# Optimization experiments

Hardware: AMD Instinct MI355X
Metric: run time of the kernel (lower is better)

The kernel has to match this reference:

```python
import jax, jax.numpy as jnp
import numpy as np

B, W, Q = 64, 128, 256
H, A, C = 512, 128, 20
SCALE = 0.05  # keep gates out of saturation


def setup_inputs() -> dict:
    key = jax.random.key(0)
    ks = jax.random.split(key, 9)
    return {
        "quantized_repr": jax.random.normal(ks[0], (B, W, Q), jnp.float32),
        "w_in": jax.random.normal(ks[1], (H, Q), jnp.float32) * SCALE,
        "b_in": jax.random.normal(ks[2], (H,), jnp.float32) * SCALE,
        "w_ih": jax.random.normal(ks[3], (4 * H, A), jnp.float32) * SCALE,
        "w_hh": jax.random.normal(ks[4], (4 * H, H), jnp.float32) * SCALE,
        "b_ih": jax.random.normal(ks[5], (4 * H,), jnp.float32) * SCALE,
        "b_hh": jax.random.normal(ks[6], (4 * H,), jnp.float32) * SCALE,
        "w_out": jax.random.normal(ks[7], (A, H), jnp.float32) * SCALE,
        "b_out": jax.random.normal(ks[8], (A,), jnp.float32) * SCALE,
        "max_char_len": C,
    }


def reference(quantized_repr, w_in, b_in, w_ih, w_hh, b_ih, b_hh, w_out, b_out, max_char_len):
    b, w, q = quantized_repr.shape
    hdim = w_hh.shape[1]
    vocab = w_out.shape[0]
    dt = quantized_repr.dtype

    # input_projection -> initial hidden, zero cell, flattened over (B*W)
    h0 = (quantized_repr @ w_in.T + b_in).reshape(b * w, hdim)
    c0 = jnp.zeros_like(h0)
    x0 = jax.nn.one_hot(jnp.zeros((b * w,), jnp.int32), vocab, dtype=dt)  # <start> = char 0
    bias = b_ih + b_hh

    def step(carry, _):
        h, c, x = carry
        gates = x @ w_ih.T + h @ w_hh.T + bias  # [BW, 4H]
        i, f, g, o = jnp.split(gates, 4, axis=-1)  # torch gate order i,f,g,o
        i = jax.nn.sigmoid(i)
        f = jax.nn.sigmoid(f)
        g = jnp.tanh(g)
        o = jax.nn.sigmoid(o)
        c = f * c + i * g
        h = o * jnp.tanh(c)
        logits = h @ w_out.T + b_out  # [BW, A]
        x_next = jax.nn.one_hot(jnp.argmax(logits, axis=-1), vocab, dtype=dt)
        return (h, c, x_next), logits

    _, logits = jax.lax.scan(step, (h0, c0, x0), None, length=max_char_len)  # [C, BW, A]
    return logits.transpose(1, 0, 2).reshape(b, w, max_char_len, vocab)
```

## Files before the change

### kernel.cpp

```cpp
#include <hip/hip_runtime.h>
#include <math.h>

typedef float fv4 __attribute__((ext_vector_type(4)));

#define NSTEP 20
#define HD 512
#define QD 256
#define VOC 128
#define RB 16
#define TPB 512

#define WG_OFF   0
#define WIH_OFF  1048576
#define WIN_OFF  1310720
#define WOUT_OFF 1441792

__device__ __forceinline__ float sig_np(float x) {
  float t = (float)exp(-(double)x);
  return __fdiv_rn(1.0f, __fadd_rn(1.0f, t));
}
__device__ __forceinline__ float tanh_np(float x) {
  return (float)tanh((double)x);
}

__global__ void repack_kernel(const float* __restrict__ w_in,
                              const float* __restrict__ w_ih,
                              const float* __restrict__ w_hh,
                              const float* __restrict__ w_out,
                              float* __restrict__ ws) {
  int t = blockIdx.x * blockDim.x + threadIdx.x;
  {
    int ki = t & 3, u = (t >> 2) & 511, g = (t >> 11) & 3, kb = t >> 13;
    ws[WG_OFF + t] = w_hh[(size_t)(g * HD + u) * HD + kb * 4 + ki];
  }
  if (t < 262144) {
    int u = t & 511, g = (t >> 9) & 3, x = t >> 11;
    ws[WIH_OFF + t] = w_ih[(size_t)(g * HD + u) * VOC + x];
  }
  if (t < 131072) {
    int ki = t & 3, u = (t >> 2) & 511, kb = t >> 11;
    ws[WIN_OFF + t] = w_in[(size_t)u * QD + kb * 4 + ki];
  }
  if (t < 65536) {
    int ki = t & 3, v = (t >> 2) & 127, kb = t >> 9;
    ws[WOUT_OFF + t] = w_out[(size_t)v * HD + kb * 4 + ki];
  }
}

__global__ __launch_bounds__(TPB, 2)
void decoder_fast(const float* __restrict__ quant,
                  const float* __restrict__ b_in,
                  const float* __restrict__ b_ih,
                  const float* __restrict__ b_hh,
                  const float* __restrict__ b_out,
                  const float* __restrict__ ws,
                  float* __restrict__ out) {
  __shared__ __align__(16) float hLDS[RB * HD];
  __shared__ __align__(16) float scratch[RB * QD];
  __shared__ int idxLDS[RB];

  const int tid  = threadIdx.x;
  const int row0 = blockIdx.x * RB;

  const fv4* Wg4   = (const fv4*)(ws + WG_OFF);
  const float* Wih = ws + WIH_OFF;
  const fv4* Win4  = (const fv4*)(ws + WIN_OFF);
  const fv4* Wout4 = (const fv4*)(ws + WOUT_OFF);
  const fv4* hLDS4 = (const fv4*)hLDS;
  const fv4* q4    = (const fv4*)scratch;

  {
    const fv4* src = (const fv4*)(quant + (size_t)row0 * QD);
    fv4* dst = (fv4*)scratch;
    dst[tid]       = src[tid];
    dst[tid + TPB] = src[tid + TPB];
  }
  if (tid < RB) idxLDS[tid] = 0;

  float bias[4];
#pragma unroll
  for (int g = 0; g < 4; ++g)
    bias[g] = __fadd_rn(b_ih[g * HD + tid], b_hh[g * HD + tid]);
  const float bout = b_out[tid & (VOC - 1)];
  const float binu = b_in[tid];

  __syncthreads();

  {
    float a[RB];
#pragma unroll
    for (int r = 0; r < RB; ++r) a[r] = 0.0f;
    for (int kb = 0; kb < QD / 4; ++kb) {
      fv4 w = Win4[kb * 512 + tid];
#pragma unroll
      for (int r = 0; r < RB; ++r) {
        fv4 qv = q4[r * 64 + kb];
        a[r] = __builtin_fmaf(w[0], qv[0], a[r]);
        a[r] = __builtin_fmaf(w[1], qv[1], a[r]);
        a[r] = __builtin_fmaf(w[2], qv[2], a[r]);
        a[r] = __builtin_fmaf(w[3], qv[3], a[r]);
      }
    }
#pragma unroll
    for (int r = 0; r < RB; ++r) hLDS[r * HD + tid] = __fadd_rn(a[r], binu);
  }

  float c[RB];
#pragma unroll
  for (int r = 0; r < RB; ++r) c[r] = 0.0f;

  __syncthreads();

  for (int t = 0; t < NSTEP; ++t) {
    float acc[RB][4];
#pragma unroll
    for (int r = 0; r < RB; ++r)
#pragma unroll
      for (int g = 0; g < 4; ++g) acc[r][g] = 0.0f;

    for (int kb = 0; kb < HD / 4; ++kb) {
      fv4 wv[4];
#pragma unroll
      for (int g = 0; g < 4; ++g) wv[g] = Wg4[(kb * 4 + g) * 512 + tid];
#pragma unroll
      for (int r = 0; r < RB; ++r) {
        fv4 hv = hLDS4[r * 128 + kb];
#pragma unroll
        for (int g = 0; g < 4; ++g) {
          acc[r][g] = __builtin_fmaf(wv[g][0], hv[0], acc[r][g]);
          acc[r][g] = __builtin_fmaf(wv[g][1], hv[1], acc[r][g]);
          acc[r][g] = __builtin_fmaf(wv[g][2], hv[2], acc[r][g]);
          acc[r][g] = __builtin_fmaf(wv[g][3], hv[3], acc[r][g]);
        }
      }
    }

    float hnew[RB];
#pragma unroll
    for (int r = 0; r < RB; ++r) {
      int ix = idxLDS[r];
      float ga[4];
#pragma unroll
      for (int g = 0; g < 4; ++g) {
        float t1 = Wih[(ix * 4 + g) * 512 + tid];
        ga[g] = __fadd_rn(__fadd_rn(t1, acc[r][g]), bias[g]);
      }
      float ig = sig_np(ga[0]);
      float fg = sig_np(ga[1]);
      float gg = tanh_np(ga[2]);
      float og = sig_np(ga[3]);
      c[r] = __fadd_rn(__fmul_rn(fg, c[r]), __fmul_rn(ig, gg));
      hnew[r] = __fmul_rn(og, tanh_np(c[r]));
    }
    __syncthreads();
#pragma unroll
    for (int r = 0; r < RB; ++r) hLDS[r * HD + tid] = hnew[r];
    __syncthreads();

    {
      int v = tid & (VOC - 1), rq = tid >> 7;
      float la[4];
#pragma unroll
      for (int j = 0; j < 4; ++j) la[j] = 0.0f;
      for (int kb = 0; kb < HD / 4; ++kb) {
        fv4 wv = Wout4[kb * 128 + v];
#pragma unroll
        for (int j = 0; j < 4; ++j) {
          fv4 hv = hLDS4[(rq * 4 + j) * 128 + kb];
          la[j] = __builtin_fmaf(wv[0], hv[0], la[j]);
          la[j] = __builtin_fmaf(wv[1], hv[1], la[j]);
          la[j] = __builtin_fmaf(wv[2], hv[2], la[j]);
          la[j] = __builtin_fmaf(wv[3], hv[3], la[j]);
        }
      }
      float* lg = scratch;
#pragma unroll
      for (int j = 0; j < 4; ++j) {
        int r = rq * 4 + j;
        float val = __fadd_rn(la[j], bout);
        lg[r * VOC + v] = val;
        out[(size_t)((row0 + r) * NSTEP + t) * VOC + v] = val;
      }
    }
    __syncthreads();

    if (tid < RB) {
      const float* lg = scratch + tid * VOC;
      float mv = lg[0];
      int mi = 0;
      for (int v = 1; v < VOC; ++v) {
        float x = lg[v];
        if (x > mv) { mv = x; mi = v; }
      }
      idxLDS[tid] = mi;
    }
    __syncthreads();
  }
}

extern "C" void kernel_launch(void* const* d_in, const int* in_sizes, int n_in,
                              void* d_out, int out_size, void* d_ws, size_t ws_size,
                              hipStream_t stream) {
  const float* quant = (const float*)d_in[0];
  const float* w_in  = (const float*)d_in[1];
  const float* b_in  = (const float*)d_in[2];
  const float* w_ih  = (const float*)d_in[3];
  const float* w_hh  = (const float*)d_in[4];
  const float* b_ih  = (const float*)d_in[5];
  const float* b_hh  = (const float*)d_in[6];
  const float* w_out = (const float*)d_in[7];
  const float* b_out = (const float*)d_in[8];
  float* out = (float*)d_out;
  float* ws  = (float*)d_ws;

  repack_kernel<<<4096, 256, 0, stream>>>(w_in, w_ih, w_hh, w_out, ws);
  decoder_fast<<<8192 / RB, TPB, 0, stream>>>(quant, b_in, b_ih, b_hh, b_out,
                                              ws, out);
}
```

Measured before the change: 7.098 ms.

## Fuse output projection into next step's gate GEMM and use wave-shuffle argmax

The kernel computes the logits for step t-1 inside the step-t gate matmul loop, since both read the same h vectors from LDS, which removes a separate pass over hLDS and two barriers per step. Argmax becomes a 64-lane shuffle reduction per wave, with a two-wave candidate merge through LDS, replacing a serial 128-element scan by 16 threads. Most of the cell state moves from registers to LDS (14 rows in LDS, 2 in registers) to cut register pressure, and the row order is rotated per thread group to spread LDS accesses. Biases are reloaded every step and a final logits pass is added after the loop; the extra LDS traffic for c and the larger loop body may offset the savings.

Measured after the change: 5.993 ms. -15.6%, faster.

```diff
diff --git a/kernel.cpp b/kernel.cpp
--- a/kernel.cpp
+++ b/kernel.cpp
@@ -9,6 +9,8 @@
 #define VOC 128
 #define RB 16
 #define TPB 512
+#define CREG 2
+#define CLDSROWS (RB - CREG)
 
 #define WG_OFF   0
 #define WIH_OFF  1048576
@@ -56,145 +58,168 @@
                   const float* __restrict__ ws,
                   float* __restrict__ out) {
   __shared__ __align__(16) float hLDS[RB * HD];
-  __shared__ __align__(16) float scratch[RB * QD];
-  __shared__ int idxLDS[RB];
+  __shared__ __align__(16) float cLDS[CLDSROWS * HD];
+  __shared__ float2 cand[RB][2];
 
   const int tid  = threadIdx.x;
   const int row0 = blockIdx.x * RB;
+  const int v    = tid & (VOC - 1);
+  const int rqs  = (tid >> 7) << 2;
+  const int wpar = (tid >> 6) & 1;
 
   const fv4* Wg4   = (const fv4*)(ws + WG_OFF);
   const float* Wih = ws + WIH_OFF;
   const fv4* Win4  = (const fv4*)(ws + WIN_OFF);
   const fv4* Wout4 = (const fv4*)(ws + WOUT_OFF);
   const fv4* hLDS4 = (const fv4*)hLDS;
-  const fv4* q4    = (const fv4*)scratch;
 
   {
     const fv4* src = (const fv4*)(quant + (size_t)row0 * QD);
-    fv4* dst = (fv4*)scratch;
+    fv4* dst = (fv4*)hLDS;
     dst[tid]       = src[tid];
     dst[tid + TPB] = src[tid + TPB];
   }
-  if (tid < RB) idxLDS[tid] = 0;
-
-  float bias[4];
-#pragma unroll
-  for (int g = 0; g < 4; ++g)
-    bias[g] = __fadd_rn(b_ih[g * HD + tid], b_hh[g * HD + tid]);
-  const float bout = b_out[tid & (VOC - 1)];
-  const float binu = b_in[tid];
-
   __syncthreads();
 
-  {
-    float a[RB];
-#pragma unroll
-    for (int r = 0; r < RB; ++r) a[r] = 0.0f;
+  float a0[RB];
+  {
+    const fv4* q4 = (const fv4*)hLDS;
+#pragma unroll
+    for (int r = 0; r < RB; ++r) a0[r] = 0.0f;
     for (int kb = 0; kb < QD / 4; ++kb) {
       fv4 w = Win4[kb * 512 + tid];
 #pragma unroll
       for (int r = 0; r < RB; ++r) {
         fv4 qv = q4[r * 64 + kb];
-        a[r] = __builtin_fmaf(w[0], qv[0], a[r]);
-        a[r] = __builtin_fmaf(w[1], qv[1], a[r]);
-        a[r] = __builtin_fmaf(w[2], qv[2], a[r]);
-        a[r] = __builtin_fmaf(w[3], qv[3], a[r]);
-      }
-    }
-#pragma unroll
-    for (int r = 0; r < RB; ++r) hLDS[r * HD + tid] = __fadd_rn(a[r], binu);
-  }
-
-  float c[RB];
-#pragma unroll
-  for (int r = 0; r < RB; ++r) c[r] = 0.0f;
-
+        a0[r] = __builtin_fmaf(w[0], qv[0], a0[r]);
+        a0[r] = __builtin_fmaf(w[1], qv[1], a0[r]);
+        a0[r] = __builtin_fmaf(w[2], qv[2], a0[r]);
+        a0[r] = __builtin_fmaf(w[3], qv[3], a0[r]);
+      }
+    }
+  }
+  const float binu = b_in[tid];
   __syncthreads();
+#pragma unroll
+  for (int r = 0; r < RB; ++r) hLDS[r * HD + tid] = __fadd_rn(a0[r], binu);
+  __syncthreads();
+
+  float cR0 = 0.0f, cR1 = 0.0f;
 
   for (int t = 0; t < NSTEP; ++t) {
     float acc[RB][4];
-#pragma unroll
-    for (int r = 0; r < RB; ++r)
-#pragma unroll
-      for (int g = 0; g < 4; ++g) acc[r][g] = 0.0f;
+    float la[4];
+#pragma unroll
+    for (int rr = 0; rr < RB; ++rr)
+#pragma unroll
+      for (int g = 0; g < 4; ++g) acc[rr][g] = 0.0f;
+#pragma unroll
+    for (int j = 0; j < 4; ++j) la[j] = 0.0f;
 
     for (int kb = 0; kb < HD / 4; ++kb) {
       fv4 wv[4];
 #pragma unroll
       for (int g = 0; g < 4; ++g) wv[g] = Wg4[(kb * 4 + g) * 512 + tid];
-#pragma unroll
-      for (int r = 0; r < RB; ++r) {
+      fv4 wvo = Wout4[kb * 128 + v];
+#pragma unroll
+      for (int rr = 0; rr < RB; ++rr) {
+        const int r = (rr + rqs) & (RB - 1);
         fv4 hv = hLDS4[r * 128 + kb];
 #pragma unroll
         for (int g = 0; g < 4; ++g) {
-          acc[r][g] = __builtin_fmaf(wv[g][0], hv[0], acc[r][g]);
-          acc[r][g] = __builtin_fmaf(wv[g][1], hv[1], acc[r][g]);
-          acc[r][g] = __builtin_fmaf(wv[g][2], hv[2], acc[r][g]);
-          acc[r][g] = __builtin_fmaf(wv[g][3], hv[3], acc[r][g]);
+          acc[rr][g] = __builtin_fmaf(wv[g][0], hv[0], acc[rr][g]);
+          acc[rr][g] = __builtin_fmaf(wv[g][1], hv[1], acc[rr][g]);
+          acc[rr][g] = __builtin_fmaf(wv[g][2], hv[2], acc[rr][g]);
+          acc[rr][g] = __builtin_fmaf(wv[g][3], hv[3], acc[rr][g]);
         }
-      }
-    }
-
-    float hnew[RB];
-#pragma unroll
-    for (int r = 0; r < RB; ++r) {
-      int ix = idxLDS[r];
+        if (rr < 4) {
+          la[rr] = __builtin_fmaf(wvo[0], hv[0], la[rr]);
+          la[rr] = __builtin_fmaf(wvo[1], hv[1], la[rr]);
+          la[rr] = __builtin_fmaf(wvo[2], hv[2], la[rr]);
+          la[rr] = __builtin_fmaf(wvo[3], hv[3], la[rr]);
+        }
+      }
+    }
+
+    if (t > 0) {
+      const float boutv = b_out[v];
+#pragma unroll
+      for (int j = 0; j < 4; ++j) {
+        float val = __fadd_rn(la[j], boutv);
+        out[(size_t)((row0 + rqs + j) * NSTEP + (t - 1)) * VOC + v] = val;
+        float mv = val;
+        int   mi = v;
+#pragma unroll
+        for (int m = 1; m < 64; m <<= 1) {
+          float ov = __shfl_xor(mv, m);
+          int   oi = __shfl_xor(mi, m);
+          bool take = (ov > mv) || (ov == mv && oi < mi);
+          mv = take ? ov : mv;
+          mi = take ? oi : mi;
+        }
+        if ((tid & 63) == 0)
+          cand[rqs + j][wpar] = make_float2(mv, __int_as_float(mi));
+      }
+    }
+    __syncthreads();
+
+    float biasg[4];
+#pragma unroll
+    for (int g = 0; g < 4; ++g)
+      biasg[g] = __fadd_rn(b_ih[g * HD + tid], b_hh[g * HD + tid]);
+
+#pragma unroll
+    for (int rr = 0; rr < RB; ++rr) {
+      const int r = (rr + rqs) & (RB - 1);
+      int ix = 0;
+      if (t > 0) {
+        float2 c0 = cand[r][0], c1 = cand[r][1];
+        ix = (c1.x > c0.x) ? __float_as_int(c1.y) : __float_as_int(c0.y);
+      }
       float ga[4];
 #pragma unroll
       for (int g = 0; g < 4; ++g) {
         float t1 = Wih[(ix * 4 + g) * 512 + tid];
-        ga[g] = __fadd_rn(__fadd_rn(t1, acc[r][g]), bias[g]);
+        ga[g] = __fadd_rn(__fadd_rn(t1, acc[rr][g]), biasg[g]);
       }
       float ig = sig_np(ga[0]);
       float fg = sig_np(ga[1]);
       float gg = tanh_np(ga[2]);
       float og = sig_np(ga[3]);
-      c[r] = __fadd_rn(__fmul_rn(fg, c[r]), __fmul_rn(ig, gg));
-      hnew[r] = __fmul_rn(og, tanh_np(c[r]));
+      float cold;
+      if (rr == RB - 2)      cold = cR0;
+      else if (rr == RB - 1) cold = cR1;
+      else                   cold = cLDS[rr * HD + tid];
+      if (t == 0) cold = 0.0f;
+      float cn = __fadd_rn(__fmul_rn(fg, cold), __fmul_rn(ig, gg));
+      if (rr == RB - 2)      cR0 = cn;
+      else if (rr == RB - 1) cR1 = cn;
+      else                   cLDS[rr * HD + tid] = cn;
+      hLDS[r * HD + tid] = __fmul_rn(og, tanh_np(cn));
     }
     __syncthreads();
-#pragma unroll
-    for (int r = 0; r < RB; ++r) hLDS[r * HD + tid] = hnew[r];
-    __syncthreads();
-
-    {
-      int v = tid & (VOC - 1), rq = tid >> 7;
-      float la[4];
-#pragma unroll
-      for (int j = 0; j < 4; ++j) la[j] = 0.0f;
-      for (int kb = 0; kb < HD / 4; ++kb) {
-        fv4 wv = Wout4[kb * 128 + v];
-#pragma unroll
-        for (int j = 0; j < 4; ++j) {
-          fv4 hv = hLDS4[(rq * 4 + j) * 128 + kb];
-          la[j] = __builtin_fmaf(wv[0], hv[0], la[j]);
-          la[j] = __builtin_fmaf(wv[1], hv[1], la[j]);
-          la[j] = __builtin_fmaf(wv[2], hv[2], la[j]);
-          la[j] = __builtin_fmaf(wv[3], hv[3], la[j]);
-        }
-      }
-      float* lg = scratch;
+  }
+
+  {
+    float la2[4];
+#pragma unroll
+    for (int j = 0; j < 4; ++j) la2[j] = 0.0f;
+    for (int kb = 0; kb < HD / 4; ++kb) {
+      fv4 wvo = Wout4[kb * 128 + v];
 #pragma unroll
       for (int j = 0; j < 4; ++j) {
-        int r = rq * 4 + j;
-        float val = __fadd_rn(la[j], bout);
-        lg[r * VOC + v] = val;
-        out[(size_t)((row0 + r) * NSTEP + t) * VOC + v] = val;
-      }
-    }
-    __syncthreads();
-
-    if (tid < RB) {
-      const float* lg = scratch + tid * VOC;
-      float mv = lg[0];
-      int mi = 0;
-      for (int v = 1; v < VOC; ++v) {
-        float x = lg[v];
-        if (x > mv) { mv = x; mi = v; }
-      }
-      idxLDS[tid] = mi;
-    }
-    __syncthreads();
+        fv4 hv = hLDS4[(rqs + j) * 128 + kb];
+        la2[j] = __builtin_fmaf(wvo[0], hv[0], la2[j]);
+        la2[j] = __builtin_fmaf(wvo[1], hv[1], la2[j]);
+        la2[j] = __builtin_fmaf(wvo[2], hv[2], la2[j]);
+        la2[j] = __builtin_fmaf(wvo[3], hv[3], la2[j]);
+      }
+    }
+    const float boutv = b_out[v];
+#pragma unroll
+    for (int j = 0; j < 4; ++j)
+      out[(size_t)((row0 + rqs + j) * NSTEP + (NSTEP - 1)) * VOC + v] =
+          __fadd_rn(la2[j], boutv);
   }
 }
 
```
